# Kernel tuning notes

Measured on AMD Instinct MI355X. Metric: run time of the kernel, lower is better.

Reference implementation:

```python
import jax, jax.numpy as jnp
import numpy as np

V, E, H, T = 8000, 256, 256, 4  # vocab, embed, lstm hidden, tagset (BMES)
B, S = 64, 512


def setup_inputs() -> dict:
    key = jax.random.key(0)
    ks = jax.random.split(key, 16)
    w = lambda k, shape, s=0.05: (jax.random.normal(k, shape, jnp.float32) * s)
    return {
        "sentence": jax.random.randint(ks[0], (B, S), 0, V),
        "tags": jax.random.randint(ks[1], (B, S), 0, T),
        "length_list": jnp.full((B,), S, dtype=jnp.int32),
        "emb": w(ks[2], (V, E), 0.1),
        "Wih_f": w(ks[3], (4 * H, E)), "Whh_f": w(ks[4], (4 * H, H)), "b_f": jnp.zeros((4 * H,), jnp.float32),
        "Wih_b": w(ks[5], (4 * H, E)), "Whh_b": w(ks[6], (4 * H, H)), "b_b": jnp.zeros((4 * H,), jnp.float32),
        "Wlin": w(ks[7], (T, 2 * H), 0.05), "blin": jnp.zeros((T,), jnp.float32),
        "start_trans": w(ks[8], (T,), 0.1), "end_trans": w(ks[9], (T,), 0.1),
        "transitions": w(ks[10], (T, T), 0.1),
    }


def _lstm_dir(xs, Wih, Whh, b, reverse):
    # xs: [S, B, E] time-major; PyTorch gate order i,f,g,o
    Bv, Hh = xs.shape[1], Whh.shape[1]
    def step(carry, x):
        h, c = carry
        g = x @ Wih.T + h @ Whh.T + b
        i, f, gg, o = jnp.split(g, 4, axis=-1)
        c = jax.nn.sigmoid(f) * c + jax.nn.sigmoid(i) * jnp.tanh(gg)
        h = jax.nn.sigmoid(o) * jnp.tanh(c)
        return (h, c), h
    init = (jnp.zeros((Bv, Hh), xs.dtype), jnp.zeros((Bv, Hh), xs.dtype))
    _, hs = jax.lax.scan(step, init, xs, reverse=reverse)
    return hs  # [S, B, H]


def _crf_llh(emis, tagsT, start, end, trans):
    # emis: [S, B, T] time-major; tagsT: [S, B]. No mask (matches original call).
    e_sc = jnp.take_along_axis(emis, tagsT[:, :, None], axis=2)[..., 0]  # [S, B]
    tr_sc = trans[tagsT[:-1], tagsT[1:]]                                  # [S-1, B]
    num = start[tagsT[0]] + e_sc.sum(0) + tr_sc.sum(0) + end[tagsT[-1]]   # [B]
    alpha = start[None, :] + emis[0]                                      # [B, T]
    def step(alpha, e):
        return jax.nn.logsumexp(alpha[:, :, None] + trans[None], axis=1) + e, None
    alpha, _ = jax.lax.scan(step, alpha, emis[1:])
    denom = jax.nn.logsumexp(alpha + end[None, :], axis=1)                # [B]
    return num - denom


def _viterbi(emis, start, end, trans):
    # emis: [S, B, T] -> best tag path [B, S]
    score = start[None, :] + emis[0]                                      # [B, T]
    def step(score, e):
        cand = score[:, :, None] + trans[None]                            # [B, T_prev, T_next]
        bp = jnp.argmax(cand, axis=1)                                     # [B, T]
        return jnp.max(cand, axis=1) + e, bp
    score, bps = jax.lax.scan(step, score, emis[1:])                      # bps: [S-1, B, T]
    last = jnp.argmax(score + end[None, :], axis=1)                       # [B]
    def back(tag, bp):
        prev = jnp.take_along_axis(bp, tag[:, None], axis=1)[:, 0]
        return prev, prev
    _, path = jax.lax.scan(back, last, bps, reverse=True)                 # [S-1, B]
    return jnp.concatenate([path, last[None]], axis=0).T                  # [B, S]


def reference(sentence, tags, length_list, emb, Wih_f, Whh_f, b_f,
              Wih_b, Whh_b, b_b, Wlin, blin, start_trans, end_trans, transitions):
    xs = jnp.swapaxes(emb[sentence], 0, 1)                                # [S, B, E]
    hf = _lstm_dir(xs, Wih_f, Whh_f, b_f, reverse=False)
    hb = _lstm_dir(xs, Wih_b, Whh_b, b_b, reverse=True)
    h = jnp.concatenate([hf, hb], axis=-1)                                # [S, B, 2H] (dropout = eval identity)
    emis = h @ Wlin.T + blin                                              # [S, B, T]
    loss = -jnp.sum(_crf_llh(emis, tags.T, start_trans, end_trans, transitions))
    tag_seq = _viterbi(emis, start_trans, end_trans, transitions)
    return tag_seq, loss
```

## Files before the change

kernel.cpp:

```cpp
#include <hip/hip_runtime.h>
#include <math.h>

#define Vv 8000
#define Ee 256
#define Hh 256
#define Tt 4
#define Bb 64
#define Ss 512

#define EPROJ_PER_DIR (Vv * 1024)
#define WMAT_PER_DIR  (Ee * 1024)

#define NSTAT 18
#define NSTRM 14
#define STAT_U32 (NSTAT * 512 * 4)

__device__ __forceinline__ float sigm(float x) { return 1.f / (1.f + expf(-x)); }

#if defined(__has_builtin)
# if __has_builtin(__builtin_amdgcn_sdot4)
#  define HAS_SDOT4 1
# endif
#endif

__device__ __forceinline__ int dot4i8(unsigned a, unsigned b, int c) {
#ifdef HAS_SDOT4
    return __builtin_amdgcn_sdot4((int)a, (int)b, c, false);
#else
    int s = c;
    #pragma unroll
    for (int i = 0; i < 4; ++i) {
        const int xa = ((int)(a << (24 - 8 * i))) >> 24;
        const int xb = ((int)(b << (24 - 8 * i))) >> 24;
        s += xa * xb;
    }
    return s;
#endif
}

__global__ void prep1_kernel(const float* __restrict__ Wih_f, const float* __restrict__ b_f,
                             const float* __restrict__ Wih_b, const float* __restrict__ b_b,
                             const float* __restrict__ Wlin,
                             float* __restrict__ WihP, float* __restrict__ bP,
                             float* __restrict__ WlinQ)
{
    int tid = blockIdx.x * blockDim.x + threadIdx.x;
    int dir = tid >> 18;
    int r   = tid & 262143;
    int k   = r >> 10;
    int jp  = r & 1023;
    int u   = jp >> 2;
    int g   = jp & 3;
    int row = g * 256 + u;
    const float* Wih = dir ? Wih_b : Wih_f;
    const float* bv  = dir ? b_b   : b_f;
    WihP[dir * WMAT_PER_DIR + k * 1024 + jp] = Wih[row * 256 + k];
    if (r < 1024) {
        bP[dir * 1024 + jp] = bv[row];
        int uu = r >> 2, tt = r & 3;
        WlinQ[(dir * 256 + uu) * 4 + tt] = Wlin[tt * (2 * Hh) + dir * 256 + uu];
    }
}

__global__ __launch_bounds__(256) void scale_kernel(const float* __restrict__ Whh_f,
                                                    const float* __restrict__ Whh_b,
                                                    float* __restrict__ scales)
{
    const int gw = blockIdx.x * 4 + (threadIdx.x >> 6);
    const int lane = threadIdx.x & 63;
    const int dir = gw >> 10;
    const int row = gw & 1023;
    const float* W = dir ? Whh_b : Whh_f;
    const float* src = W + (size_t)row * 256 + lane * 4;
    float m = fmaxf(fmaxf(fabsf(src[0]), fabsf(src[1])),
                    fmaxf(fabsf(src[2]), fabsf(src[3])));
    #pragma unroll
    for (int off = 32; off > 0; off >>= 1) m = fmaxf(m, __shfl_down(m, off));
    if (lane == 0) scales[gw] = fmaxf(m, 1e-12f) / 127.f;
}

__global__ __launch_bounds__(256) void quant_kernel(const float* __restrict__ Whh_f,
                                                    const float* __restrict__ Whh_b,
                                                    const float* __restrict__ scales,
                                                    unsigned int* __restrict__ W8)
{
    const int idx = blockIdx.x * 256 + threadIdx.x;
    const int dir = idx >> 16;
    const int rem = idx & 65535;
    int slot, t, j, kw;
    if (rem < STAT_U32) {
        slot = rem >> 11; const int r2 = rem & 2047; t = r2 >> 2; j = r2 & 3;
        kw = 2 * slot + (j >> 1);
    } else {
        const int q2 = rem - STAT_U32;
        slot = q2 >> 11; const int r2 = q2 & 2047; t = r2 >> 2; j = r2 & 3;
        kw = 36 + 2 * slot + (j >> 1);
    }
    const int rr = j & 1;
    const int u = t & 255;
    const int gs = (t < 256 ? 0 : 2) + rr;
    const int row = gs * 256 + u;
    const float* W = dir ? Whh_b : Whh_f;
    const float sc = scales[dir * 1024 + row];
    const float inv = 1.f / sc;
    unsigned int v = 0;
    #pragma unroll
    for (int i = 0; i < 4; ++i) {
        const float w = W[(size_t)row * 256 + kw * 4 + i];
        int q = (int)rintf(w * inv);
        q = q > 127 ? 127 : (q < -127 ? -127 : q);
        v |= ((unsigned int)(unsigned char)(signed char)q) << (8 * i);
    }
    W8[idx] = v;
}

#define BM 64
#define BN 128
#define BK 16
__global__ __launch_bounds__(256) void embproj_gemm(const float* __restrict__ emb,
                                                    const float* __restrict__ WihP,
                                                    const float* __restrict__ bP,
                                                    float* __restrict__ embproj)
{
    int dir = blockIdx.z;
    const float* Bmat = WihP + dir * WMAT_PER_DIR;
    float* C = embproj + (size_t)dir * EPROJ_PER_DIR;
    int m0 = blockIdx.x * BM;
    int n0 = blockIdx.y * BN;

    __shared__ float As[BK][BM];
    __shared__ float Bs[BK][BN];

    int t = threadIdx.x;
    int tm = (t & 15) * 4;
    int tn = (t >> 4) * 8;
    float acc[4][8];
    #pragma unroll
    for (int i = 0; i < 4; ++i)
        #pragma unroll
        for (int j = 0; j < 8; ++j) acc[i][j] = 0.f;

    for (int k0 = 0; k0 < Ee; k0 += BK) {
        {
            int row = t >> 2, seg = t & 3;
            float4 a4 = *(const float4*)(&emb[(size_t)(m0 + row) * Ee + k0 + seg * 4]);
            As[seg * 4 + 0][row] = a4.x;
            As[seg * 4 + 1][row] = a4.y;
            As[seg * 4 + 2][row] = a4.z;
            As[seg * 4 + 3][row] = a4.w;
        }
        {
            int kk = t >> 4, nn = (t & 15) * 8;
            float4 b0 = *(const float4*)(&Bmat[(size_t)(k0 + kk) * 1024 + n0 + nn]);
            float4 b1 = *(const float4*)(&Bmat[(size_t)(k0 + kk) * 1024 + n0 + nn + 4]);
            *(float4*)&Bs[kk][nn]     = b0;
            *(float4*)&Bs[kk][nn + 4] = b1;
        }
        __syncthreads();
        #pragma unroll
        for (int k = 0; k < BK; ++k) {
            float4 a  = *(const float4*)&As[k][tm];
            float4 b0 = *(const float4*)&Bs[k][tn];
            float4 b1 = *(const float4*)&Bs[k][tn + 4];
            float av[4] = {a.x, a.y, a.z, a.w};
            float bv[8] = {b0.x, b0.y, b0.z, b0.w, b1.x, b1.y, b1.z, b1.w};
            #pragma unroll
            for (int i = 0; i < 4; ++i)
                #pragma unroll
                for (int j = 0; j < 8; ++j)
                    acc[i][j] += av[i] * bv[j];
        }
        __syncthreads();
    }
    #pragma unroll
    for (int i = 0; i < 4; ++i) {
        int m = m0 + tm + i;
        #pragma unroll
        for (int j = 0; j < 8; j += 4) {
            float4 o;
            o.x = acc[i][j + 0] + bP[dir * 1024 + n0 + tn + j + 0];
            o.y = acc[i][j + 1] + bP[dir * 1024 + n0 + tn + j + 1];
            o.z = acc[i][j + 2] + bP[dir * 1024 + n0 + tn + j + 2];
            o.w = acc[i][j + 3] + bP[dir * 1024 + n0 + tn + j + 3];
            *(float4*)&C[(size_t)m * 1024 + n0 + tn + j] = o;
        }
    }
}

__global__ __attribute__((amdgpu_flat_work_group_size(512, 512)))
__attribute__((amdgpu_waves_per_eu(2, 2))) void lstm_stream_kernel(
    const int* __restrict__ sentence,
    const float* __restrict__ embproj,
    const unsigned int* __restrict__ W8,
    const float* __restrict__ scales,
    const float* __restrict__ WlinQ,
    float* __restrict__ emisP)
{
    extern __shared__ char smem[];
    uint4*        SWl   = (uint4*)smem;
    unsigned int* h8    = (unsigned int*)(smem + 147456);
    float2*       part  = (float2*)(smem + 147456 + 256);
    float4*       emred = (float4*)(smem + 147456 + 256 + 2048);

    const int bx  = blockIdx.x;
    const int dir = bx >> 6;
    const int b   = bx & 63;
    const int t   = threadIdx.x;
    const int lane = t & 63, wv = t >> 6;
    const int u   = t & 255;
    const bool lo = (t < 256);
    const int gs0 = lo ? 0 : 2;

    const unsigned int* Wd   = W8 + (size_t)dir * 65536;
    const unsigned int* Wstr = Wd + STAT_U32;

    #pragma unroll
    for (int i = 0; i < NSTAT; ++i)
        SWl[i * 512 + t] = *(const uint4*)(Wd + (size_t)(i * 512 + t) * 4);
    if (t < 64) h8[t] = 0u;

    const float sc0 = scales[dir * 1024 + gs0 * 256 + u] * (1.f / 127.f);
    const float sc1 = scales[dir * 1024 + (gs0 + 1) * 256 + u] * (1.f / 127.f);
    float4 wl = make_float4(0.f, 0.f, 0.f, 0.f);
    if (lo) wl = *(const float4*)&WlinQ[(dir * 256 + u) * 4];
    const float* EP = embproj + (size_t)dir * EPROJ_PER_DIR;
    const int* sent = sentence + (size_t)b * Ss;
    float c = 0.f;

    __syncthreads();

    for (int s = 0; s < Ss; ++s) {
        const int pos = dir ? (Ss - 1 - s) : s;
        const int tok = sent[pos];
        const float2 ep = *(const float2*)(EP + (size_t)tok * 1024 + u * 4 + gs0);

        uint4 sb[NSTRM];
        #pragma unroll
        for (int i = 0; i < NSTRM; ++i)
            sb[i] = *(const uint4*)(Wstr + (size_t)(i * 512 + t) * 4);

        int a0 = 0, a1 = 0;
        #pragma unroll
        for (int i = 0; i < NSTAT; ++i) {
            const uint4 w = SWl[i * 512 + t];
            const uint2 hw = *(const uint2*)&h8[2 * i];
            a0 = dot4i8(w.x, hw.x, a0); a1 = dot4i8(w.y, hw.x, a1);
            a0 = dot4i8(w.z, hw.y, a0); a1 = dot4i8(w.w, hw.y, a1);
        }
        #pragma unroll
        for (int i = 0; i < NSTRM; ++i) {
            const uint4 w = sb[i];
            const uint2 hw = *(const uint2*)&h8[36 + 2 * i];
            a0 = dot4i8(w.x, hw.x, a0); a1 = dot4i8(w.y, hw.x, a1);
            a0 = dot4i8(w.z, hw.y, a0); a1 = dot4i8(w.w, hw.y, a1);
        }

        const float g0 = (float)a0 * sc0 + ep.x;
        const float g1 = (float)a1 * sc1 + ep.y;
        if (!lo) part[u] = make_float2(g0, g1);
        __syncthreads();

        if (lo) {
            const float2 pg = part[u];
            c = sigm(g1) * c + sigm(g0) * tanhf(pg.x);
            const float h = sigm(pg.y) * tanhf(c);
            float4 em = make_float4(h * wl.x, h * wl.y, h * wl.z, h * wl.w);
            #pragma unroll
            for (int off = 32; off > 0; off >>= 1) {
                em.x += __shfl_down(em.x, off); em.y += __shfl_down(em.y, off);
                em.z += __shfl_down(em.z, off); em.w += __shfl_down(em.w, off);
            }
            if (lane == 0) emred[wv] = em;
            ((char*)h8)[u] = (char)(int)rintf(h * 127.f);
        }
        __syncthreads();

        if (t == 0) {
            const float4 e0 = emred[0], e1 = emred[1], e2 = emred[2], e3 = emred[3];
            float4 o;
            o.x = e0.x + e1.x + e2.x + e3.x;
            o.y = e0.y + e1.y + e2.y + e3.y;
            o.z = e0.z + e1.z + e2.z + e3.z;
            o.w = e0.w + e1.w + e2.w + e3.w;
            *(float4*)&emisP[(((size_t)dir * Ss + pos) * Bb + b) * 4] = o;
        }
    }
}

#define EM2(S_, B_, J_) (emisA[(((size_t)(S_)) * Bb + (B_)) * 4 + (J_)] + \
                         emisB[(((size_t)(S_)) * Bb + (B_)) * 4 + (J_)])

__global__ __launch_bounds__(64) void tail_kernel(
    const float* __restrict__ emisA, const float* __restrict__ emisB,
    const float* __restrict__ blin, const float* __restrict__ start_t,
    const float* __restrict__ end_t, const float* __restrict__ trans,
    const int* __restrict__ tags, float* __restrict__ out_tags,
    float* __restrict__ out_loss)
{
    const int blk = blockIdx.x;
    const int t = threadIdx.x;
    const int b_loc = t >> 2, j = t & 3;
    const int base = t & ~3;

    if (blk < 4) {
        __shared__ unsigned char bp_sh[16][513][4];
        __shared__ unsigned char tag_sh[16][520];
        const int b = blk * 16 + b_loc;
        const float trj0 = trans[0*4+j], trj1 = trans[1*4+j],
                    trj2 = trans[2*4+j], trj3 = trans[3*4+j];
        const float blj = blin[j];
        float score = start_t[j] + EM2(0, b, j) + blj;
        for (int s = 1; s < Ss; ++s) {
            const float e = EM2(s, b, j) + blj;
            const float s0 = __shfl(score, base+0), s1 = __shfl(score, base+1),
                        s2 = __shfl(score, base+2), s3 = __shfl(score, base+3);
            float best = s0 + trj0; int bi = 0;
            float v = s1 + trj1; if (v > best) { best = v; bi = 1; }
            v = s2 + trj2; if (v > best) { best = v; bi = 2; }
            v = s3 + trj3; if (v > best) { best = v; bi = 3; }
            score = best + e;
            bp_sh[b_loc][s][j] = (unsigned char)bi;
        }
        const float fv = score + end_t[j];
        const float f0 = __shfl(fv, base+0), f1 = __shfl(fv, base+1),
                    f2 = __shfl(fv, base+2), f3 = __shfl(fv, base+3);
        __syncthreads();
        if (j == 0) {
            float best = f0; int tag = 0;
            if (f1 > best) { best = f1; tag = 1; }
            if (f2 > best) { best = f2; tag = 2; }
            if (f3 > best) { best = f3; tag = 3; }
            tag_sh[b_loc][Ss-1] = (unsigned char)tag;
            for (int s = Ss - 1; s >= 1; --s) {
                tag = bp_sh[b_loc][s][tag];
                tag_sh[b_loc][s-1] = (unsigned char)tag;
            }
        }
        __syncthreads();
        for (int idx = t; idx < 16 * Ss; idx += 64) {
            const int bl = idx >> 9, s = idx & (Ss - 1);
            out_tags[(size_t)(blk*16 + bl) * Ss + s] = (float)tag_sh[bl][s];
        }
    } else {
        const int b = (blk - 4) * 16 + b_loc;
        const float trj0 = trans[0*4+j], trj1 = trans[1*4+j],
                    trj2 = trans[2*4+j], trj3 = trans[3*4+j];
        const float blj = blin[j];
        float alpha = start_t[j] + EM2(0, b, j) + blj;
        for (int s = 1; s < Ss; ++s) {
            const float e = EM2(s, b, j) + blj;
            const float a0 = __shfl(alpha, base+0), a1 = __shfl(alpha, base+1),
                        a2 = __shfl(alpha, base+2), a3 = __shfl(alpha, base+3);
            const float x0 = a0 + trj0, x1 = a1 + trj1, x2 = a2 + trj2, x3 = a3 + trj3;
            const float m = fmaxf(fmaxf(x0, x1), fmaxf(x2, x3));
            alpha = m + logf(expf(x0-m) + expf(x1-m) + expf(x2-m) + expf(x3-m)) + e;
        }
        const float dv = alpha + end_t[j];
        const float d0 = __shfl(dv, base+0), d1 = __shfl(dv, base+1),
                    d2 = __shfl(dv, base+2), d3 = __shfl(dv, base+3);
        const float dm = fmaxf(fmaxf(d0, d1), fmaxf(d2, d3));
        const float denom = dm + logf(expf(d0-dm) + expf(d1-dm) + expf(d2-dm) + expf(d3-dm));

        const int lo = j * 128, hi = lo + 128;
        float num = 0.f;
        int tprev = (lo > 0) ? tags[(size_t)b*Ss + lo - 1] : 0;
        if (j == 0) num += start_t[tags[(size_t)b*Ss]];
        if (j == 3) num += end_t[tags[(size_t)b*Ss + Ss - 1]];
        for (int s = lo; s < hi; ++s) {
            const int tg = tags[(size_t)b*Ss + s];
            num += EM2(s, b, tg) + blin[tg];
            if (s > 0) num += trans[tprev*4 + tg];
            tprev = tg;
        }
        num += __shfl_xor(num, 1);
        num += __shfl_xor(num, 2);
        float lb = (j == 0) ? (denom - num) : 0.f;
        #pragma unroll
        for (int off = 32; off > 0; off >>= 1) lb += __shfl_down(lb, off);
        if (t == 0) atomicAdd(out_loss, lb);
    }
}

extern "C" void kernel_launch(void* const* d_in, const int* in_sizes, int n_in,
                              void* d_out, int out_size, void* d_ws, size_t ws_size,
                              hipStream_t stream)
{
    const int*   sentence = (const int*)d_in[0];
    const int*   tags     = (const int*)d_in[1];
    const float* emb      = (const float*)d_in[3];
    const float* Wih_f    = (const float*)d_in[4];
    const float* Whh_f    = (const float*)d_in[5];
    const float* b_f      = (const float*)d_in[6];
    const float* Wih_b    = (const float*)d_in[7];
    const float* Whh_b    = (const float*)d_in[8];
    const float* b_b      = (const float*)d_in[9];
    const float* Wlin     = (const float*)d_in[10];
    const float* blin     = (const float*)d_in[11];
    const float* start_t  = (const float*)d_in[12];
    const float* end_t    = (const float*)d_in[13];
    const float* trans    = (const float*)d_in[14];

    float*        embproj = (float*)d_ws;
    float*        WihP    = embproj + 2 * EPROJ_PER_DIR;
    float*        bP      = WihP + 2 * WMAT_PER_DIR;
    float*        WlinQ   = bP + 2048;
    float*        scales  = WlinQ + 2048;
    unsigned int* W8      = (unsigned int*)(scales + 2048);
    float*        emisP   = (float*)(W8 + 131072);
    float*        emisA   = emisP;
    float*        emisB   = emisP + Ss * Bb * 4;

    prep1_kernel<<<2048, 256, 0, stream>>>(Wih_f, b_f, Wih_b, b_b, Wlin,
                                           WihP, bP, WlinQ);
    scale_kernel<<<512, 256, 0, stream>>>(Whh_f, Whh_b, scales);
    quant_kernel<<<512, 256, 0, stream>>>(Whh_f, Whh_b, scales, W8);

    dim3 gg(Vv / BM, 1024 / BN, 2);
    embproj_gemm<<<gg, 256, 0, stream>>>(emb, WihP, bP, embproj);

    lstm_stream_kernel<<<128, 512, 149824, stream>>>(sentence, embproj, W8,
                                                     scales, WlinQ, emisP);

    float* out = (float*)d_out;
    float* out_loss = out + Bb * Ss;
    hipMemsetAsync(out_loss, 0, sizeof(float), stream);
    tail_kernel<<<8, 64, 0, stream>>>(emisA, emisB, blin, start_t, end_t, trans,
                                      tags, out, out_loss);
}
```

Measured before the change: 1.096 ms.

## Move emission projection off critical path with int8 dot in spare wave

Emission output is no longer reduced in float by the four gate-update waves followed by a thread-0 store after the barrier. Wave 4 now computes it one step late from the quantized h8 with int8 dot products, and the last step is handled after the loop. This removes one shuffle reduction and a serial store from each recurrent step. Hidden-state words are also broadcast with readlane from one register load instead of shared-memory reads per iteration, and accumulation is split into two chains for ILP. Emissions now use quantized h and Wlin, which adds precision error.

```diff
diff --git a/kernel.cpp b/kernel.cpp
--- a/kernel.cpp
+++ b/kernel.cpp
@@ -114,6 +114,32 @@
     W8[idx] = v;
 }
 
+__global__ __launch_bounds__(512) void wl8_kernel(const float* __restrict__ Wlin,
+                                                  unsigned int* __restrict__ wl8T,
+                                                  float* __restrict__ scfac)
+{
+    const int w = threadIdx.x >> 6;
+    const int lane = threadIdx.x & 63;
+    const int dir = w >> 2, t = w & 3;
+    const float4 v = *(const float4*)(Wlin + t * (2 * Hh) + dir * 256 + lane * 4);
+    float m = fmaxf(fmaxf(fabsf(v.x), fabsf(v.y)), fmaxf(fabsf(v.z), fabsf(v.w)));
+    #pragma unroll
+    for (int off = 32; off > 0; off >>= 1) m = fmaxf(m, __shfl_down(m, off));
+    const float mall = __builtin_amdgcn_readfirstlane(m);
+    const float sc = fmaxf(mall, 1e-12f) / 127.f;
+    const float inv = 1.f / sc;
+    const float vv[4] = {v.x, v.y, v.z, v.w};
+    unsigned int pk = 0;
+    #pragma unroll
+    for (int i = 0; i < 4; ++i) {
+        int q = (int)rintf(vv[i] * inv);
+        q = q > 127 ? 127 : (q < -127 ? -127 : q);
+        pk |= ((unsigned int)(unsigned char)(signed char)q) << (8 * i);
+    }
+    wl8T[w * 64 + lane] = pk;
+    if (lane == 0) scfac[w] = sc / 127.f;
+}
+
 #define BM 64
 #define BN 128
 #define BK 16
@@ -193,14 +219,14 @@
     const float* __restrict__ embproj,
     const unsigned int* __restrict__ W8,
     const float* __restrict__ scales,
-    const float* __restrict__ WlinQ,
+    const unsigned int* __restrict__ wl8T,
+    const float* __restrict__ scfac,
     float* __restrict__ emisP)
 {
     extern __shared__ char smem[];
     uint4*        SWl   = (uint4*)smem;
     unsigned int* h8    = (unsigned int*)(smem + 147456);
     float2*       part  = (float2*)(smem + 147456 + 256);
-    float4*       emred = (float4*)(smem + 147456 + 256 + 2048);
 
     const int bx  = blockIdx.x;
     const int dir = bx >> 6;
@@ -221,11 +247,19 @@
 
     const float sc0 = scales[dir * 1024 + gs0 * 256 + u] * (1.f / 127.f);
     const float sc1 = scales[dir * 1024 + (gs0 + 1) * 256 + u] * (1.f / 127.f);
-    float4 wl = make_float4(0.f, 0.f, 0.f, 0.f);
-    if (lo) wl = *(const float4*)&WlinQ[(dir * 256 + u) * 4];
     const float* EP = embproj + (size_t)dir * EPROJ_PER_DIR;
     const int* sent = sentence + (size_t)b * Ss;
     float c = 0.f;
+
+    unsigned int wlq0 = 0, wlq1 = 0, wlq2 = 0, wlq3 = 0;
+    float4 efac = make_float4(0.f, 0.f, 0.f, 0.f);
+    if (wv == 4) {
+        wlq0 = wl8T[(dir * 4 + 0) * 64 + lane];
+        wlq1 = wl8T[(dir * 4 + 1) * 64 + lane];
+        wlq2 = wl8T[(dir * 4 + 2) * 64 + lane];
+        wlq3 = wl8T[(dir * 4 + 3) * 64 + lane];
+        efac = *(const float4*)&scfac[dir * 4];
+    }
 
     __syncthreads();
 
@@ -234,26 +268,60 @@
         const int tok = sent[pos];
         const float2 ep = *(const float2*)(EP + (size_t)tok * 1024 + u * 4 + gs0);
 
+        const int v_h = (int)h8[lane];
+
         uint4 sb[NSTRM];
         #pragma unroll
         for (int i = 0; i < NSTRM; ++i)
             sb[i] = *(const uint4*)(Wstr + (size_t)(i * 512 + t) * 4);
 
-        int a0 = 0, a1 = 0;
+        if (wv == 4 && s > 0) {
+            int e0 = dot4i8(wlq0, (unsigned)v_h, 0);
+            int e1 = dot4i8(wlq1, (unsigned)v_h, 0);
+            int e2 = dot4i8(wlq2, (unsigned)v_h, 0);
+            int e3 = dot4i8(wlq3, (unsigned)v_h, 0);
+            #pragma unroll
+            for (int off = 32; off > 0; off >>= 1) {
+                e0 += __shfl_down(e0, off); e1 += __shfl_down(e1, off);
+                e2 += __shfl_down(e2, off); e3 += __shfl_down(e3, off);
+            }
+            if (lane == 0) {
+                const int pp = dir ? (Ss - s) : (s - 1);
+                float4 o;
+                o.x = (float)e0 * efac.x; o.y = (float)e1 * efac.y;
+                o.z = (float)e2 * efac.z; o.w = (float)e3 * efac.w;
+                *(float4*)&emisP[(((size_t)dir * Ss + pp) * Bb + b) * 4] = o;
+            }
+        }
+
+        int a0e = 0, a1e = 0, a0o = 0, a1o = 0;
         #pragma unroll
         for (int i = 0; i < NSTAT; ++i) {
             const uint4 w = SWl[i * 512 + t];
-            const uint2 hw = *(const uint2*)&h8[2 * i];
-            a0 = dot4i8(w.x, hw.x, a0); a1 = dot4i8(w.y, hw.x, a1);
-            a0 = dot4i8(w.z, hw.y, a0); a1 = dot4i8(w.w, hw.y, a1);
+            const unsigned h0 = (unsigned)__builtin_amdgcn_readlane(v_h, 2 * i);
+            const unsigned h1 = (unsigned)__builtin_amdgcn_readlane(v_h, 2 * i + 1);
+            if (i & 1) {
+                a0o = dot4i8(w.x, h0, a0o); a1o = dot4i8(w.y, h0, a1o);
+                a0o = dot4i8(w.z, h1, a0o); a1o = dot4i8(w.w, h1, a1o);
+            } else {
+                a0e = dot4i8(w.x, h0, a0e); a1e = dot4i8(w.y, h0, a1e);
+                a0e = dot4i8(w.z, h1, a0e); a1e = dot4i8(w.w, h1, a1e);
+            }
         }
         #pragma unroll
         for (int i = 0; i < NSTRM; ++i) {
             const uint4 w = sb[i];
-            const uint2 hw = *(const uint2*)&h8[36 + 2 * i];
-            a0 = dot4i8(w.x, hw.x, a0); a1 = dot4i8(w.y, hw.x, a1);
-            a0 = dot4i8(w.z, hw.y, a0); a1 = dot4i8(w.w, hw.y, a1);
-        }
+            const unsigned h0 = (unsigned)__builtin_amdgcn_readlane(v_h, 36 + 2 * i);
+            const unsigned h1 = (unsigned)__builtin_amdgcn_readlane(v_h, 37 + 2 * i);
+            if (i & 1) {
+                a0o = dot4i8(w.x, h0, a0o); a1o = dot4i8(w.y, h0, a1o);
+                a0o = dot4i8(w.z, h1, a0o); a1o = dot4i8(w.w, h1, a1o);
+            } else {
+                a0e = dot4i8(w.x, h0, a0e); a1e = dot4i8(w.y, h0, a1e);
+                a0e = dot4i8(w.z, h1, a0e); a1e = dot4i8(w.w, h1, a1e);
+            }
+        }
+        const int a0 = a0e + a0o, a1 = a1e + a1o;
 
         const float g0 = (float)a0 * sc0 + ep.x;
         const float g1 = (float)a1 * sc1 + ep.y;
@@ -264,25 +332,28 @@
             const float2 pg = part[u];
             c = sigm(g1) * c + sigm(g0) * tanhf(pg.x);
             const float h = sigm(pg.y) * tanhf(c);
-            float4 em = make_float4(h * wl.x, h * wl.y, h * wl.z, h * wl.w);
-            #pragma unroll
-            for (int off = 32; off > 0; off >>= 1) {
-                em.x += __shfl_down(em.x, off); em.y += __shfl_down(em.y, off);
-                em.z += __shfl_down(em.z, off); em.w += __shfl_down(em.w, off);
-            }
-            if (lane == 0) emred[wv] = em;
             ((char*)h8)[u] = (char)(int)rintf(h * 127.f);
         }
         __syncthreads();
-
-        if (t == 0) {
-            const float4 e0 = emred[0], e1 = emred[1], e2 = emred[2], e3 = emred[3];
+    }
+
+    if (wv == 4) {
+        const int v_h = (int)h8[lane];
+        int e0 = dot4i8(wlq0, (unsigned)v_h, 0);
+        int e1 = dot4i8(wlq1, (unsigned)v_h, 0);
+        int e2 = dot4i8(wlq2, (unsigned)v_h, 0);
+        int e3 = dot4i8(wlq3, (unsigned)v_h, 0);
+        #pragma unroll
+        for (int off = 32; off > 0; off >>= 1) {
+            e0 += __shfl_down(e0, off); e1 += __shfl_down(e1, off);
+            e2 += __shfl_down(e2, off); e3 += __shfl_down(e3, off);
+        }
+        if (lane == 0) {
+            const int pp = dir ? 0 : (Ss - 1);
             float4 o;
-            o.x = e0.x + e1.x + e2.x + e3.x;
-            o.y = e0.y + e1.y + e2.y + e3.y;
-            o.z = e0.z + e1.z + e2.z + e3.z;
-            o.w = e0.w + e1.w + e2.w + e3.w;
-            *(float4*)&emisP[(((size_t)dir * Ss + pos) * Bb + b) * 4] = o;
+            o.x = (float)e0 * efac.x; o.y = (float)e1 * efac.y;
+            o.z = (float)e2 * efac.z; o.w = (float)e3 * efac.w;
+            *(float4*)&emisP[(((size_t)dir * Ss + pp) * Bb + b) * 4] = o;
         }
     }
 }
@@ -406,7 +477,9 @@
     float*        WlinQ   = bP + 2048;
     float*        scales  = WlinQ + 2048;
     unsigned int* W8      = (unsigned int*)(scales + 2048);
-    float*        emisP   = (float*)(W8 + 131072);
+    unsigned int* wl8T    = W8 + 131072;
+    float*        scfac   = (float*)(wl8T + 512);
+    float*        emisP   = scfac + 56;
     float*        emisA   = emisP;
     float*        emisB   = emisP + Ss * Bb * 4;
 
@@ -414,12 +487,13 @@
                                            WihP, bP, WlinQ);
     scale_kernel<<<512, 256, 0, stream>>>(Whh_f, Whh_b, scales);
     quant_kernel<<<512, 256, 0, stream>>>(Whh_f, Whh_b, scales, W8);
+    wl8_kernel<<<1, 512, 0, stream>>>(Wlin, wl8T, scfac);
 
     dim3 gg(Vv / BM, 1024 / BN, 2);
     embproj_gemm<<<gg, 256, 0, stream>>>(emb, WihP, bP, embproj);
 
-    lstm_stream_kernel<<<128, 512, 149824, stream>>>(sentence, embproj, W8,
-                                                     scales, WlinQ, emisP);
+    lstm_stream_kernel<<<128, 512, 149760, stream>>>(sentence, embproj, W8,
+                                                     scales, wl8T, scfac, emisP);
 
     float* out = (float*)d_out;
     float* out_loss = out + Bb * Ss;
```

Measured after the change: 1.064 ms. -3.0%, faster.
